# Kernel tuning notes

Measured on AMD Instinct MI355X. Metric: run time of the kernel, lower is better.

## Reference

```python
import jax, jax.numpy as jnp
import numpy as np

N_CLASSES = 2
N_FEATURES = 100
PSI_DIM = 10
BATCH = 500000


def setup_inputs() -> dict:
    key = jax.random.key(0)
    k_x, k_ar, k_ai, k_pr, k_pi = jax.random.split(key, 5)
    x = jax.random.normal(k_x, (BATCH, N_FEATURES), dtype=jnp.float32)
    A_real = jax.random.normal(k_ar, (N_CLASSES, PSI_DIM, PSI_DIM, N_FEATURES), dtype=jnp.float32)
    A_imag = jax.random.normal(k_ai, (N_CLASSES, PSI_DIM, PSI_DIM, N_FEATURES), dtype=jnp.float32)
    psi_real = jax.random.normal(k_pr, (PSI_DIM,), dtype=jnp.float32)
    psi_imag = jax.random.normal(k_pi, (PSI_DIM,), dtype=jnp.float32)
    return {"x": x, "A_real": A_real, "A_imag": A_imag, "psi_real": psi_real, "psi_imag": psi_imag}


def reference(x, A_real, A_imag, psi_real, psi_imag):
    # result_{tk} = Re[ sum_{i,j,a} conj(psi)_i A_{kija} x_{ta} psi_j ]  (x is real)
    # P_{ij} = conj(psi)_i psi_j ; expand in real arithmetic to avoid complex tensors.
    P_re = jnp.outer(psi_real, psi_real) + jnp.outer(psi_imag, psi_imag)   # [i,j]
    P_im = jnp.outer(psi_real, psi_imag) - jnp.outer(psi_imag, psi_real)   # [i,j]
    # Re(M)_{ka} = sum_{ij} P_re A_real - P_im A_imag  -> tiny [2,100] matrix
    M_re = jnp.einsum('ij,kija->ka', P_re, A_real) - jnp.einsum('ij,kija->ka', P_im, A_imag)
    # out_{tk} = sum_a x_{ta} Re(M)_{ka} : memory-bound [t,100] x [100,2]
    return jnp.einsum('ta,ka->tk', x, M_re)
```

## Files before the change

### kernel.cpp

```cpp
#include <hip/hip_runtime.h>

#define NF      100
#define BLOCK   128
#define TILE    32
#define F4T     (TILE * 25)
#define NLD     7
#define F4PAD   (NLD * BLOCK)
#define NBUF    3
#define MAXGRID 768

__device__ __forceinline__ void stage_tile(const float4* __restrict__ x4,
                                           float4* dst, int f4base, int maxf4,
                                           int tid) {
#pragma unroll
  for (int u = 0; u < NLD; ++u) {
    int idx = u * BLOCK + tid;
    int g = f4base + (idx < F4T ? idx : 0);
    g = g > maxf4 ? maxf4 : g;
    __builtin_amdgcn_global_load_lds(
        (const __attribute__((address_space(1))) void*)(x4 + g),
        (__attribute__((address_space(3))) void*)(dst + idx),
        16, 0, 0);
  }
}

#define WAITCNT_VM8_NOLGKM 0x0F78

__global__ __launch_bounds__(BLOCK, 1) void fused_kernel(
    const float4* __restrict__ x4,
    const float* __restrict__ A_real, const float* __restrict__ A_imag,
    const float* __restrict__ psi_real, const float* __restrict__ psi_imag,
    float2* __restrict__ out, int batch, int ntiles) {
  __shared__ float4 xs[NBUF][F4PAD];
  __shared__ __align__(16) float2 msl[NF];

  const int tid = threadIdx.x;
  const int maxf4 = batch * 25 - 1;
  const int stride = gridDim.x;

  float4* b0 = &xs[0][0];
  float4* b1 = &xs[1][0];
  float4* b2 = &xs[2][0];

  int t = blockIdx.x;
  stage_tile(x4, b0, t * F4T, maxf4, tid);
  stage_tile(x4, b1, (t + stride) * F4T, maxf4, tid);

  if (tid < NF) {
    const int a = tid;
    float pr[10], pi[10];
#pragma unroll
    for (int i = 0; i < 10; ++i) { pr[i] = psi_real[i]; pi[i] = psi_imag[i]; }
    float m0 = 0.f, m1 = 0.f;
#pragma unroll
    for (int i = 0; i < 10; ++i) {
#pragma unroll
      for (int j = 0; j < 10; ++j) {
        float pre = pr[i] * pr[j] + pi[i] * pi[j];
        float pim = pr[i] * pi[j] - pi[i] * pr[j];
        int off = (i * 10 + j) * NF + a;
        m0 = fmaf(pre, A_real[off], m0);
        m0 = fmaf(-pim, A_imag[off], m0);
        m1 = fmaf(pre, A_real[off + 10000], m1);
        m1 = fmaf(-pim, A_imag[off + 10000], m1);
      }
    }
    msl[a] = make_float2(m0, m1);
  }
  __syncthreads();

  const int q = tid & 3;
  const int r = tid >> 2;
  const float4* msl4 = (const float4*)msl;
  float4 mreg[14];
#pragma unroll
  for (int i = 0; i < 7; ++i) {
    int j = q + 4 * i;
    int jc = j < 25 ? j : 24;
    mreg[2 * i]     = msl4[2 * jc];
    mreg[2 * i + 1] = msl4[2 * jc + 1];
  }

  for (; t < ntiles; t += stride) {
    __builtin_amdgcn_s_waitcnt(WAITCNT_VM8_NOLGKM);
    __builtin_amdgcn_s_barrier();

    stage_tile(x4, b2, (t + 2 * stride) * F4T, maxf4, tid);

    const float4* xrow = b0 + r * 25 + q;
    float a0 = 0.f, a1 = 0.f;
#pragma unroll
    for (int i = 0; i < 7; ++i) {
      if (i < 6 || q == 0) {
        float4 xv = xrow[4 * i];
        float4 mA = mreg[2 * i];
        float4 mB = mreg[2 * i + 1];
        a0 = fmaf(xv.x, mA.x, a0); a1 = fmaf(xv.x, mA.y, a1);
        a0 = fmaf(xv.y, mA.z, a0); a1 = fmaf(xv.y, mA.w, a1);
        a0 = fmaf(xv.z, mB.x, a0); a1 = fmaf(xv.z, mB.y, a1);
        a0 = fmaf(xv.w, mB.z, a0); a1 = fmaf(xv.w, mB.w, a1);
      }
    }
    a0 += __shfl_xor(a0, 1); a0 += __shfl_xor(a0, 2);
    a1 += __shfl_xor(a1, 1); a1 += __shfl_xor(a1, 2);
    const int t0 = t * TILE;
    if (q == 0 && r < batch - t0) out[t0 + r] = make_float2(a0, a1);

    float4* tmp = b0; b0 = b1; b1 = b2; b2 = tmp;
  }
}

extern "C" void kernel_launch(void* const* d_in, const int* in_sizes, int n_in,
                              void* d_out, int out_size, void* d_ws, size_t ws_size,
                              hipStream_t stream) {
  const float* x  = (const float*)d_in[0];
  const float* Ar = (const float*)d_in[1];
  const float* Ai = (const float*)d_in[2];
  const float* pr = (const float*)d_in[3];
  const float* pi = (const float*)d_in[4];
  const int batch = in_sizes[0] / NF;

  const int ntiles = (batch + TILE - 1) / TILE;
  const int grid = ntiles < MAXGRID ? ntiles : MAXGRID;
  fused_kernel<<<grid, BLOCK, 0, stream>>>(
      (const float4*)x, Ar, Ai, pr, pi, (float2*)d_out, batch, ntiles);
}
```

Before: 288.0 us.

## Replace triple-buffered LDS staging with direct global float4 loads per row

```diff
diff --git a/kernel.cpp b/kernel.cpp
--- a/kernel.cpp
+++ b/kernel.cpp
@@ -1,50 +1,19 @@
 #include <hip/hip_runtime.h>
 
 #define NF      100
-#define BLOCK   128
-#define TILE    32
-#define F4T     (TILE * 25)
-#define NLD     7
-#define F4PAD   (NLD * BLOCK)
-#define NBUF    3
-#define MAXGRID 768
+#define BLOCK   256
+#define RPB     64
+#define MAXGRID 1024
 
-__device__ __forceinline__ void stage_tile(const float4* __restrict__ x4,
-                                           float4* dst, int f4base, int maxf4,
-                                           int tid) {
-#pragma unroll
-  for (int u = 0; u < NLD; ++u) {
-    int idx = u * BLOCK + tid;
-    int g = f4base + (idx < F4T ? idx : 0);
-    g = g > maxf4 ? maxf4 : g;
-    __builtin_amdgcn_global_load_lds(
-        (const __attribute__((address_space(1))) void*)(x4 + g),
-        (__attribute__((address_space(3))) void*)(dst + idx),
-        16, 0, 0);
-  }
-}
-
-#define WAITCNT_VM8_NOLGKM 0x0F78
 
 __global__ __launch_bounds__(BLOCK, 1) void fused_kernel(
     const float4* __restrict__ x4,
     const float* __restrict__ A_real, const float* __restrict__ A_imag,
     const float* __restrict__ psi_real, const float* __restrict__ psi_imag,
-    float2* __restrict__ out, int batch, int ntiles) {
-  __shared__ float4 xs[NBUF][F4PAD];
+    float2* __restrict__ out, int batch, int nslabs) {
   __shared__ __align__(16) float2 msl[NF];
 
   const int tid = threadIdx.x;
-  const int maxf4 = batch * 25 - 1;
-  const int stride = gridDim.x;
-
-  float4* b0 = &xs[0][0];
-  float4* b1 = &xs[1][0];
-  float4* b2 = &xs[2][0];
-
-  int t = blockIdx.x;
-  stage_tile(x4, b0, t * F4T, maxf4, tid);
-  stage_tile(x4, b1, (t + stride) * F4T, maxf4, tid);
 
   if (tid < NF) {
     const int a = tid;
@@ -81,18 +50,16 @@
     mreg[2 * i + 1] = msl4[2 * jc + 1];
   }
 
-  for (; t < ntiles; t += stride) {
-    __builtin_amdgcn_s_waitcnt(WAITCNT_VM8_NOLGKM);
-    __builtin_amdgcn_s_barrier();
+  for (int t = blockIdx.x; t < nslabs; t += gridDim.x) {
+    const int row = t * RPB + r;
+    const int rc  = row < batch ? row : batch - 1;
+    const float4* xr = x4 + rc * 25 + q;
 
-    stage_tile(x4, b2, (t + 2 * stride) * F4T, maxf4, tid);
-
-    const float4* xrow = b0 + r * 25 + q;
     float a0 = 0.f, a1 = 0.f;
 #pragma unroll
     for (int i = 0; i < 7; ++i) {
       if (i < 6 || q == 0) {
-        float4 xv = xrow[4 * i];
+        float4 xv = xr[4 * i];
         float4 mA = mreg[2 * i];
         float4 mB = mreg[2 * i + 1];
         a0 = fmaf(xv.x, mA.x, a0); a1 = fmaf(xv.x, mA.y, a1);
@@ -103,10 +70,7 @@
     }
     a0 += __shfl_xor(a0, 1); a0 += __shfl_xor(a0, 2);
     a1 += __shfl_xor(a1, 1); a1 += __shfl_xor(a1, 2);
-    const int t0 = t * TILE;
-    if (q == 0 && r < batch - t0) out[t0 + r] = make_float2(a0, a1);
-
-    float4* tmp = b0; b0 = b1; b1 = b2; b2 = tmp;
+    if (q == 0 && row < batch) out[row] = make_float2(a0, a1);
   }
 }
 
@@ -120,8 +84,8 @@
   const float* pi = (const float*)d_in[4];
   const int batch = in_sizes[0] / NF;
 
-  const int ntiles = (batch + TILE - 1) / TILE;
-  const int grid = ntiles < MAXGRID ? ntiles : MAXGRID;
+  const int nslabs = (batch + RPB - 1) / RPB;
+  const int grid = nslabs < MAXGRID ? nslabs : MAXGRID;
   fused_kernel<<<grid, BLOCK, 0, stream>>>(
-      (const float4*)x, Ar, Ai, pr, pi, (float2*)d_out, batch, ntiles);
+      (const float4*)x, Ar, Ai, pr, pi, (float2*)d_out, batch, nslabs);
 }
```

After: 297.7 us. +3.3%, slower.
